# Optimization experiments

Measured on AMD Instinct MI355X. Metric: run time of the kernel, lower is better.

## Reference

```python
import jax, jax.numpy as jnp
from jax import lax
import numpy as np

SIGMA = 25.0
NUM_STEPS = 100
DT = 0.01
SQRT_DT = float(np.sqrt(DT))


def _score(x, eig, t, cond, W1, we, wt, b1, Wc, W2, b2):
    # x: [B,S,H], eig: [B,S], t: scalar, cond: [B,S,H] or None
    h = x @ W1 + eig[..., None] * we + t * wt + b1
    if cond is not None:
        h = h + cond @ Wc
    h = jax.nn.silu(h)
    return h @ W2 + b2


def _diffuse(x_T, eigvals, eigvecs, cond, params, key):
    # reverse SDE from t=1 to t=0 in NUM_STEPS steps
    ts = jnp.linspace(1.0, 0.0, NUM_STEPS)
    keys = jax.random.split(key, NUM_STEPS)
    VT = jnp.swapaxes(eigvecs, -2, -1)  # [B,S,S]

    def step(x, tk):
        t, k = tk
        x_spec = VT @ x                                   # spectral projection [B,S,H]
        score = _score(x_spec, eigvals, t, cond, *params)
        drift = -(SIGMA ** (2.0 * t)) * score
        noise = jax.random.normal(k, x.shape, x.dtype)
        x_new = x - drift * DT + (SIGMA ** t) * SQRT_DT * noise
        return x_new, None

    x, _ = lax.scan(step, x_T, (ts, keys))
    return x


def _make_net(key, H, scale):
    k = jax.random.split(key, 4)
    return dict(
        W1=jax.random.normal(k[0], (H, H), jnp.float32) * scale,
        we=jax.random.normal(k[1], (H,), jnp.float32) * scale,
        wt=jax.random.normal(k[2], (H,), jnp.float32) * scale,
        b1=jnp.zeros((H,), jnp.float32),
        Wc=jax.random.normal(k[3], (H, H), jnp.float32) * scale,
        W2=jax.random.normal(jax.random.fold_in(key, 99), (H, H), jnp.float32) * scale,
        b2=jnp.zeros((H,), jnp.float32),
    )


def setup_inputs() -> dict:
    key = jax.random.key(0)
    B, S, H = 4, 512, 256
    ks = jax.random.split(key, 9)
    inp = {}
    inp['features_text'] = jax.random.normal(ks[0], (B, S, H), jnp.float32)
    inp['features_audio'] = jax.random.normal(ks[1], (B, S, H), jnp.float32)
    inp['features_visual'] = jax.random.normal(ks[2], (B, S, H), jnp.float32)
    sg = jax.random.normal(ks[3], (B, S, S), jnp.float32)
    inp['speaker_graph'] = 0.5 * (sg + jnp.swapaxes(sg, -2, -1))  # symmetric for eigh
    tg = jax.random.normal(ks[4], (B, S, S), jnp.float32)
    inp['temporal_graph'] = 0.5 * (tg + jnp.swapaxes(tg, -2, -1))
    # only text modality (index 0) is missing -> diffusion path for text only
    inp['missing_mask'] = jnp.zeros((B, S, 3), bool).at[:, :, 0].set(True)
    inp['x_T'] = jax.random.normal(ks[5], (B, S, H), jnp.float32)
    scale = 1.0 / np.sqrt(H)
    for prefix, k in [('ts', ks[6]), ('tt', ks[7])]:  # text_speaker / text_temporal nets
        net = _make_net(k, H, scale)
        for name, v in net.items():
            inp[f'{prefix}_{name}'] = v
    kr = jax.random.split(ks[8], 2)
    inp['rec_W'] = jax.random.normal(kr[0], (H, H), jnp.float32) * scale
    inp['rec_b'] = jnp.zeros((H,), jnp.float32)
    return inp


def reference(features_text, features_audio, features_visual,
              speaker_graph, temporal_graph, missing_mask, x_T,
              ts_W1, ts_we, ts_wt, ts_b1, ts_Wc, ts_W2, ts_b2,
              tt_W1, tt_we, tt_wt, tt_b1, tt_Wc, tt_W2, tt_b2,
              rec_W, rec_b):
    # spectral decomposition of both graphs
    s_vals, s_vecs = jnp.linalg.eigh(speaker_graph)
    t_vals, t_vecs = jnp.linalg.eigh(temporal_graph)

    feats = {'text': features_text, 'audio': features_audio, 'visual': features_visual}
    miss = np.asarray(missing_mask)  # concrete branching as in torch forward
    any_missing = [bool(miss[:, :, i].any()) for i in range(3)]

    params = {'text': (
        (ts_W1, ts_we, ts_wt, ts_b1, ts_Wc, ts_W2, ts_b2),
        (tt_W1, tt_we, tt_wt, tt_b1, tt_Wc, tt_W2, tt_b2))}
    key = jax.random.key(42)

    recovered = {}
    for i, modality in enumerate(['text', 'audio', 'visual']):
        if any_missing[i]:
            # condition = mean of present (non-missing) other modalities
            cond_feats = [feats[m] for j, m in enumerate(['text', 'audio', 'visual'])
                          if m != modality and not any_missing[j]]
            cond = None
            if cond_feats:
                cond = jnp.mean(jnp.stack(cond_feats, axis=-1), axis=-1)
            k_s, k_t = jax.random.split(jax.random.fold_in(key, i))
            p_s, p_t = params[modality]
            x_s = _diffuse(x_T, s_vals, s_vecs, cond, p_s, k_s)
            x_t = _diffuse(x_T, t_vals, t_vecs, cond, p_t, k_t)
            rec = 0.5 * (x_s + x_t)
            recovered[modality] = rec @ rec_W + rec_b
        else:
            recovered[modality] = feats[modality]
    return (recovered['text'], recovered['audio'], recovered['visual'])
```

## Files before the change

### kernel.cpp

```cpp
#include <hip/hip_runtime.h>
#include <math.h>
#include <stdint.h>


#define NT 256
#define SZF 131072
#define MATSZ 262144
#define NB 16
#define ILAST 384
#define TBASE (ILAST+1)
#define TSZ (512-TBASE)

#define BD_DK   0
#define BD_ZK   4096
#define BD_RZK  8192
#define BD_TAU  12288
#define BD_DS   16384
#define BD_RHO  20480
#define BD_KSK  20736
#define BD_KIDX 22784
#define BD_DIDX 24832
#define BD_PERM 26880
#define BD_CNT  28928

#define ALD(p)    __hip_atomic_load((p),  __ATOMIC_RELAXED, __HIP_MEMORY_SCOPE_AGENT)
#define AST(p,v)  __hip_atomic_store((p), (v), __ATOMIC_RELAXED, __HIP_MEMORY_SCOPE_AGENT)

__host__ __device__ static inline unsigned rotl32(unsigned v, int r){ return (v<<r)|(v>>(32-r)); }

__host__ __device__ static inline void tf2x32(unsigned k0, unsigned k1,
                                              unsigned x0, unsigned x1,
                                              unsigned* o0, unsigned* o1){
  unsigned ks2 = k0 ^ k1 ^ 0x1BD11BDAu;
  x0 += k0; x1 += k1;
#define TF4(r0,r1,r2,r3) \
  x0 += x1; x1 = rotl32(x1,r0); x1 ^= x0; \
  x0 += x1; x1 = rotl32(x1,r1); x1 ^= x0; \
  x0 += x1; x1 = rotl32(x1,r2); x1 ^= x0; \
  x0 += x1; x1 = rotl32(x1,r3); x1 ^= x0;
  TF4(13,15,26,6)  x0 += k1;  x1 += ks2 + 1u;
  TF4(17,29,16,24) x0 += ks2; x1 += k0 + 2u;
  TF4(13,15,26,6)  x0 += k0;  x1 += k1 + 3u;
  TF4(17,29,16,24) x0 += k1;  x1 += ks2 + 4u;
  TF4(13,15,26,6)  x0 += ks2; x1 += k0 + 5u;
#undef TF4
  *o0 = x0; *o1 = x1;
}

__device__ static inline float erfinv_xla(float x){
  float w = -log1pf(-x*x);
  float p;
  if (w < 5.0f){
    w -= 2.5f;
    p = 2.81022636e-08f;
    p = fmaf(p, w, 3.43273939e-07f);
    p = fmaf(p, w, -3.5233877e-06f);
    p = fmaf(p, w, -4.39150654e-06f);
    p = fmaf(p, w, 0.00021858087f);
    p = fmaf(p, w, -0.00125372503f);
    p = fmaf(p, w, -0.00417768164f);
    p = fmaf(p, w, 0.246640727f);
    p = fmaf(p, w, 1.50140941f);
  } else {
    w = sqrtf(w) - 3.0f;
    p = -0.000200214257f;
    p = fmaf(p, w, 0.000100950558f);
    p = fmaf(p, w, 0.00134934322f);
    p = fmaf(p, w, -0.00367342844f);
    p = fmaf(p, w, 0.00573950773f);
    p = fmaf(p, w, -0.0076224613f);
    p = fmaf(p, w, 0.00943887047f);
    p = fmaf(p, w, 1.00167406f);
    p = fmaf(p, w, 2.83297682f);
  }
  return p*x;
}

__device__ static inline float bits_to_normal(unsigned bits){
  const float MINV = -0.99999994f;
  float f = __uint_as_float((bits >> 9) | 0x3f800000u) - 1.0f;
  float u = fmaxf(MINV, fmaf(f, 2.0f, MINV));
  return 1.41421356237309515f * erfinv_xla(u);
}

__device__ __forceinline__ void gbar2(unsigned* slots, int sg, int g, unsigned epoch,
                                      int* sdead){
  __threadfence_block();
  __syncthreads();
  int t = threadIdx.x;
  if (t == 0) AST(slots + (sg*NB + g)*16, epoch);
  if (t < NB && !*sdead){
    unsigned* sl = slots + (sg*NB + t)*16;
    int spins = 0;
    while (ALD(sl) < epoch){
      __builtin_amdgcn_s_sleep(1);
      if (++spins > (1<<24)){ *sdead = 1; break; }
    }
  }
  __syncthreads();
}

__global__ __launch_bounds__(256) void k_sytd2_lds(const float* Gs, const float* Gt,
                                                   double* Vb, double* smalls,
                                                   unsigned* slots, double* Atail){
  int sg = blockIdx.x / NB, g = blockIdx.x % NB;
  const float* G = (sg < 4) ? (Gs + (size_t)sg*MATSZ) : (Gt + (size_t)(sg-4)*MATSZ);
  double* V = Vb + (size_t)sg*MATSZ;
  double* d  = smalls + (size_t)sg*512;
  double* e  = smalls + 4096 + (size_t)sg*512;
  double* tu = smalls + 8192 + (size_t)sg*512;
  double* acc0 = smalls + 274688 + (size_t)sg*512;
  double* acc1 = acc0 + 4096;
  double* col0 = smalls + 282880 + (size_t)sg*512;
  double* col1 = col0 + 4096;
  double* vvh  = smalls + 291072 + (size_t)sg*512;
  double* At = Atail + (size_t)sg*MATSZ;
  int t = threadIdx.x, wave = t >> 6, lane = t & 63;

  __shared__ double Arows[32][512];
  __shared__ double vv[512], wv[512], col2[512], acc[512];
  __shared__ double red[4];
  __shared__ double bc[4];
  __shared__ int sdead;

  if (t == 0) sdead = 0;

  for (int j=0; j<32; j++){
    int r = NB*j + g;
    for (int c=t; c<512; c+=256)
      Arows[j][c] = (double)G[(size_t)r*512 + c];
  }

  for (int r=t; r<512; r+=256) col2[r] = (r>=1) ? (double)G[(size_t)r*512] : 0.0;
  __syncthreads();
  {
    double part = 0.0;
    for (int r=2+t; r<512; r+=256) part += col2[r]*col2[r];
    #pragma unroll
    for (int off=32; off; off>>=1) part += __shfl_down(part, off, 64);
    if (lane==0) red[wave]=part;
    __syncthreads();
    if (t==0){
      double xsq = red[0]+red[1]+red[2]+red[3];
      double alpha = col2[1];
      double beta,tv,scal;
      if (xsq == 0.0){ beta=alpha; tv=0.0; scal=0.0; }
      else {
        beta = -copysign(sqrt(alpha*alpha + xsq), alpha);
        tv = (beta - alpha)/beta;
        scal = 1.0/(alpha - beta);
      }
      if (g==0){ e[0]=beta; tu[0]=tv; }
      bc[0]=tv; bc[1]=scal;
    }
  }
  __syncthreads();
  double tauv = bc[0];
  {
    double scal = bc[1];
    for (int r=t; r<512; r+=256){
      double v = 0.0;
      if (r==1) v = 1.0;
      else if (r>1) v = (tauv==0.0) ? 0.0 : col2[r]*scal;
      vv[r]=v;
      if (r>=1 && (r & (NB-1))==g) V[r] = v;
    }
  }
  __syncthreads();
  if (g==0){
    for (int r=1+t; r<512; r+=256) AST(&col0[r], (double)G[(size_t)r*512 + 1]);
  }
  {
    int r0 = 1 + ((g - 1) & (NB-1));
    for (int r = r0 + NB*wave; r < 512; r += 4*NB){
      const double* Ar = Arows[r>>4];
      double p = 0.0;
      for (int c=lane; c<512; c+=64) p += Ar[c]*vv[c];
      #pragma unroll
      for (int off=32; off; off>>=1) p += __shfl_down(p, off, 64);
      if (lane==0) AST(&acc0[r], p);
    }
  }

  for (int i=0; i<ILAST; i++){
    gbar2(slots, sg, g, (unsigned)(i+1), &sdead);
    int lo=i+1, lo2=i+2;
    double* accR = (i&1) ? acc1 : acc0;
    double* colR = (i&1) ? col1 : col0;
    double* accW = (i&1) ? acc0 : acc1;
    double* colW = (i&1) ? col0 : col1;
    double part = 0.0;
    for (int r=lo+t; r<512; r+=256){
      double a_ = ALD(&accR[r]);
      double c_ = ALD(&colR[r]);
      acc[r]=a_; col2[r]=c_;
      part += (tauv*a_)*vv[r];
    }
    #pragma unroll
    for (int off=32; off; off>>=1) part += __shfl_down(part, off, 64);
    if (lane==0) red[wave]=part;
    __syncthreads();
    {
      double dot = red[0]+red[1]+red[2]+red[3];
      double alpha2 = -0.5*tauv*dot;
      double vlo = vv[lo];
      double wlo = fma(alpha2, vlo, tauv*acc[lo]);
      for (int r=lo+t; r<512; r+=256){
        double wr = fma(alpha2, vv[r], tauv*acc[r]);
        wv[r]=wr;
        col2[r] = col2[r] - vv[r]*wlo - wr*vlo;
      }
    }
    __syncthreads();
    part = 0.0;
    for (int r=lo2+1+t; r<512; r+=256) part += col2[r]*col2[r];
    #pragma unroll
    for (int off=32; off; off>>=1) part += __shfl_down(part, off, 64);
    if (lane==0) red[wave]=part;
    __syncthreads();
    double tau2, scal2;
    {
      double xsq = red[0]+red[1]+red[2]+red[3];
      double alpha = col2[lo2];
      double beta;
      if (xsq == 0.0){ beta=alpha; tau2=0.0; scal2=0.0; }
      else {
        beta = -copysign(sqrt(alpha*alpha + xsq), alpha);
        tau2 = (beta - alpha)/beta;
        scal2 = 1.0/(alpha - beta);
      }
      if (t==0 && g==0){ e[lo]=beta; tu[lo]=tau2; }
    }
    {
      double vvc[8], wvc[8], v2c[8];
      #pragma unroll
      for (int j=0;j<8;j++){
        int c = lo + lane + 64*j;
        bool ok = c < 512;
        vvc[j] = ok ? vv[c] : 0.0;
        wvc[j] = ok ? wv[c] : 0.0;
        double v2v = 0.0;
        if (ok){
          if (c==lo2) v2v = 1.0;
          else if (c>lo2) v2v = (tau2==0.0) ? 0.0 : col2[c]*scal2;
        }
        v2c[j] = v2v;
      }
      int r0 = lo + ((g - lo) & (NB-1));
      for (int r = r0 + NB*wave; r < 512; r += 4*NB){
        double* Ar = Arows[r>>4];
        double vr = vv[r], wr = wv[r];
        double p = 0.0;
        #pragma unroll
        for (int j=0;j<8;j++){
          int c = lo + lane + 64*j;
          if (c < 512){
            double an = Ar[c] - vr*wvc[j] - wr*vvc[j];
            Ar[c] = an;
            p += an * v2c[j];
            if (c == lo2) AST(&colW[r], an);
          }
        }
        #pragma unroll
        for (int off=32; off; off>>=1) p += __shfl_down(p, off, 64);
        if (lane==0) AST(&accW[r], p);
      }
    }
    __syncthreads();
    for (int r=t; r<512; r+=256){
      double v = 0.0;
      if (r==lo2) v = 1.0;
      else if (r>lo2) v = (tau2==0.0) ? 0.0 : col2[r]*scal2;
      vv[r]=v;
      if (r>=lo2 && (r & (NB-1))==g) V[(size_t)lo*512 + r] = v;
    }
    tauv = tau2;
  }

  if (t < 32){
    int r = NB*t + g;
    if (r <= ILAST) d[r] = Arows[t][r];
  }
  for (int j=0; j<32; j++){
    int r = NB*j + g;
    if (r >= TBASE){
      for (int c=TBASE+t; c<512; c+=256)
        At[(size_t)r*512 + c] = Arows[j][c];
    }
  }
  if (g==0){
    for (int r=t; r<512; r+=256) vvh[r] = vv[r];
  }
}

__global__ __launch_bounds__(256) void k_sy_tail(const double* Atail, double* Vb,
                                                 double* smalls){
  int sg = blockIdx.x;
  double* V = Vb + (size_t)sg*MATSZ;
  double* d  = smalls + (size_t)sg*512;
  double* e  = smalls + 4096 + (size_t)sg*512;
  double* tu = smalls + 8192 + (size_t)sg*512;
  const double* accG = smalls + 274688 + (size_t)sg*512;
  const double* colG = smalls + 282880 + (size_t)sg*512;
  const double* vvG  = smalls + 291072 + (size_t)sg*512;
  const double* At0 = Atail + (size_t)sg*MATSZ;
  int t = threadIdx.x, wave = t >> 6, lane = t & 63;

  __shared__ double At[TSZ*128];
  __shared__ double vv[512], wv[512], col2[512], acc[512], accN[512], colN[512];
  __shared__ double red[4];

  for (int rl=0; rl<TSZ; rl++)
    for (int cl=t; cl<TSZ; cl+=256)
      At[rl*128+cl] = At0[(size_t)(TBASE+rl)*512 + TBASE+cl];
  for (int r=t; r<512; r+=256){
    if (r >= ILAST){ vv[r]=vvG[r]; acc[r]=accG[r]; col2[r]=colG[r]; }
  }
  double tauv = tu[ILAST];
  __syncthreads();

  for (int i=ILAST; i<510; i++){
    int lo=i+1, lo2=i+2;
    double part = 0.0;
    for (int r=lo+t; r<512; r+=256) part += (tauv*acc[r])*vv[r];
    #pragma unroll
    for (int off=32; off; off>>=1) part += __shfl_down(part, off, 64);
    if (lane==0) red[wave]=part;
    __syncthreads();
    {
      double dot = red[0]+red[1]+red[2]+red[3];
      double alpha2 = -0.5*tauv*dot;
      double vlo = vv[lo];
      double wlo = fma(alpha2, vlo, tauv*acc[lo]);
      for (int r=lo+t; r<512; r+=256){
        double wr = fma(alpha2, vv[r], tauv*acc[r]);
        wv[r]=wr;
        col2[r] = col2[r] - vv[r]*wlo - wr*vlo;
      }
    }
    __syncthreads();
    part = 0.0;
    for (int r=lo2+1+t; r<512; r+=256) part += col2[r]*col2[r];
    #pragma unroll
    for (int off=32; off; off>>=1) part += __shfl_down(part, off, 64);
    if (lane==0) red[wave]=part;
    __syncthreads();
    double tau2, scal2;
    {
      double xsq = red[0]+red[1]+red[2]+red[3];
      double alpha = col2[lo2];
      double beta;
      if (xsq == 0.0){ beta=alpha; tau2=0.0; scal2=0.0; }
      else {
        beta = -copysign(sqrt(alpha*alpha + xsq), alpha);
        tau2 = (beta - alpha)/beta;
        scal2 = 1.0/(alpha - beta);
      }
      if (t==0){ e[lo]=beta; tu[lo]=tau2; }
    }
    {
      double vvc[8], wvc[8], v2c[8];
      #pragma unroll
      for (int j=0;j<8;j++){
        int c = lo + lane + 64*j;
        bool ok = c < 512;
        vvc[j] = ok ? vv[c] : 0.0;
        wvc[j] = ok ? wv[c] : 0.0;
        double v2v = 0.0;
        if (ok){
          if (c==lo2) v2v = 1.0;
          else if (c>lo2) v2v = (tau2==0.0) ? 0.0 : col2[c]*scal2;
        }
        v2c[j] = v2v;
      }
      for (int r = lo + wave; r < 512; r += 4){
        double* Ar = &At[(r-TBASE)*128];
        double vr = vv[r], wr = wv[r];
        double p = 0.0;
        #pragma unroll
        for (int j=0;j<8;j++){
          int c = lo + lane + 64*j;
          if (c < 512){
            double an = Ar[c-TBASE] - vr*wvc[j] - wr*vvc[j];
            Ar[c-TBASE] = an;
            p += an * v2c[j];
            if (c == lo2) colN[r] = an;
          }
        }
        #pragma unroll
        for (int off=32; off; off>>=1) p += __shfl_down(p, off, 64);
        if (lane==0) accN[r] = p;
      }
    }
    __syncthreads();
    for (int r=t; r<512; r+=256){
      if (r >= lo2){
        double v = (r==lo2) ? 1.0 : ((tau2==0.0) ? 0.0 : col2[r]*scal2);
        vv[r]=v;
        V[(size_t)lo*512 + r] = v;
        col2[r] = colN[r];
        acc[r] = accN[r];
      }
    }
    tauv = tau2;
    __syncthreads();
  }
  for (int rl=t; rl<TSZ; rl+=256) d[TBASE+rl] = At[rl*128+rl];
}

__global__ void k_scale(double* smalls, int sbase){
  int sg = sbase + blockIdx.x, t = threadIdx.x;
  double* d = smalls + (size_t)sg*512;
  double* e = smalls + 4096 + (size_t)sg*512;
  __shared__ double red[256];
  double m = 0.0;
  for (int i=t;i<512;i+=256) m = fmax(m, fabs(d[i]));
  for (int i=t;i<511;i+=256) m = fmax(m, fabs(e[i]));
  red[t]=m; __syncthreads();
  for (int off=128; off; off>>=1){ if (t<off) red[t]=fmax(red[t],red[t+off]); __syncthreads(); }
  double org = red[0]; if (org == 0.0) org = 1.0;
  if (t==0) smalls[12288+sg] = org;
  double inv = 1.0/org;
  __syncthreads();
  for (int i=t;i<512;i+=256) d[i] *= inv;
  for (int i=t;i<511;i+=256) e[i] *= inv;
  __syncthreads();
  if (t < 31){
    int k = t + 1;
    double ae = fabs(e[16*k - 1]);
    d[16*k - 1] -= ae;
    d[16*k]     -= ae;
  }
}

__global__ __launch_bounds__(256) void k_leaves(double* smalls, double* Zb, int sbase){
  __shared__ double LA[4][256];
  __shared__ double LQ[4][256];
  int t = threadIdx.x, w = t >> 6, lane = t & 63;
  int L = blockIdx.x*4 + w;
  int s_local = L >> 5;
  int sg = sbase + s_local;
  int leaf = L & 31;
  double* dd = smalls + (size_t)sg*512;
  double* ee = smalls + 4096 + (size_t)sg*512;
  double* Z = Zb + (size_t)s_local*MATSZ;
  int base = leaf*16;
  double* A = LA[w]; double* Q = LQ[w];

  for (int i=lane; i<256; i+=64){ A[i]=0.0; Q[i]=0.0; }
  __builtin_amdgcn_sched_barrier(0);
  if (lane < 16){ A[lane*17] = dd[base+lane]; Q[lane*17] = 1.0; }
  if (lane < 15){
    double ev = ee[base+lane];
    A[lane*16+lane+1] = ev; A[(lane+1)*16+lane] = ev;
  }
  __builtin_amdgcn_sched_barrier(0);
  double nr = 0.0;
  if (lane == 0){ for (int i=0;i<256;i++) nr += A[i]*A[i]; }
  nr = __shfl(nr, 0, 64);
  double thr = nr*1e-30 + 1e-300;

  for (int sweep=0; sweep<60; sweep++){
    double offs = 0.0;
    for (int p=0;p<15;p++) for (int q=p+1;q<16;q++){
      double apq = A[p*16+q];
      offs += 2.0*apq*apq;
      if (apq == 0.0) continue;
      double theta = 0.5*(A[q*17]-A[p*17])/apq;
      double tt;
      if (fabs(theta) > 1e18) tt = 0.5/theta;
      else tt = copysign(1.0, theta)/(fabs(theta)+sqrt(theta*theta+1.0));
      double cc = 1.0/sqrt(tt*tt+1.0), ss = tt*cc;
      __builtin_amdgcn_sched_barrier(0);
      if (lane < 16){
        int k = lane;
        double akp=A[k*16+p], akq=A[k*16+q];
        A[k*16+p] = cc*akp - ss*akq;
        A[k*16+q] = ss*akp + cc*akq;
      }
      __builtin_amdgcn_sched_barrier(0);
      if (lane < 16){
        int k = lane;
        double apk=A[p*16+k], aqk=A[q*16+k];
        A[p*16+k] = cc*apk - ss*aqk;
        A[q*16+k] = ss*apk + cc*aqk;
      }
      __builtin_amdgcn_sched_barrier(0);
      if (lane < 16){
        int k = lane;
        double qkp=Q[k*16+p], qkq=Q[k*16+q];
        Q[k*16+p] = cc*qkp - ss*qkq;
        Q[k*16+q] = ss*qkp + cc*qkq;
      }
      __builtin_amdgcn_sched_barrier(0);
    }
    if (offs < thr) break;
  }
  __builtin_amdgcn_sched_barrier(0);
  if (lane == 0){
    for (int i=0;i<16;i++){
      int mi=i;
      for (int j=i+1;j<16;j++) if (A[j*17] < A[mi*17]) mi=j;
      if (mi!=i){
        double tmp=A[i*17]; A[i*17]=A[mi*17]; A[mi*17]=tmp;
        for (int k=0;k<16;k++){ double q1=Q[k*16+i]; Q[k*16+i]=Q[k*16+mi]; Q[k*16+mi]=q1; }
      }
    }
  }
  __builtin_amdgcn_sched_barrier(0);
  if (lane < 16) dd[base+lane] = A[lane*17];
  for (int i=lane; i<256; i+=64){
    int r = i >> 4, c = i & 15;
    Z[(size_t)(base+r)*512 + base + c] = Q[i];
  }
}

__global__ __launch_bounds__(256) void k_deflate(double* smalls, const double* Zsrc_b,
                                                 double* bscr, int level, int sbase){
  const double EPS32 = 5.9604644775390625e-8;
  const double ISQ2  = 0.70710678118654752440;
  int s_local = blockIdx.x;
  int sg = sbase + s_local;
  int hh = 16 << level, n = hh << 1;
  int merge = blockIdx.y, start = merge*n;
  double* d = smalls + (size_t)sg*512;
  const double* e = smalls + 4096 + (size_t)sg*512;
  const double* Z = Zsrc_b + (size_t)s_local*MATSZ;
  double* rotg = smalls + 12544 + (size_t)(sg*32+merge)*1024;
  double* dkG  = bscr + BD_DK  + (size_t)s_local*512 + start;
  double* zkG  = bscr + BD_ZK  + (size_t)s_local*512 + start;
  double* rzkG = bscr + BD_RZK + (size_t)s_local*512 + start;
  double* dsG  = bscr + BD_DS  + (size_t)s_local*512 + start;
  double* rhoG = bscr + BD_RHO;
  int* kidxG = (int*)(bscr + BD_KIDX) + s_local*512 + start;
  int* didxG = (int*)(bscr + BD_DIDX) + s_local*512 + start;
  int* permG = (int*)(bscr + BD_PERM) + s_local*512 + start;
  int* cntG  = (int*)(bscr + BD_CNT) + (s_local*32+merge)*2;

  __shared__ double ds[512], zl[512];
  __shared__ double rc[256], rs[256];
  __shared__ double red[256];
  __shared__ double sv[2];
  __shared__ int perm[512], kidx[512], didx[512];
  __shared__ int rp[256], rq[256];
  __shared__ int counts[2];
  int t = threadIdx.x;
  if (t == 0){
    int i=0, j=hh, k=0;
    while (i < hh && j < n){
      if (d[start+i] <= d[start+j]) perm[k++]=i++; else perm[k++]=j++;
    }
    while (i < hh) perm[k++]=i++;
    while (j < n)  perm[k++]=j++;
  }
  __syncthreads();
  double eb = e[start+hh-1];
  double rho = 2.0*fabs(eb);
  double sgn = (eb < 0.0) ? -1.0 : 1.0;
  for (int i=t; i<n; i+=NT){
    int p = perm[i];
    ds[i] = d[start+p];
    double zr = (p < hh) ? Z[(size_t)(start+hh-1)*512 + start + p]
                         : sgn * Z[(size_t)(start+hh)*512 + start + p];
    zl[i] = zr * ISQ2;
  }
  __syncthreads();
  double m = 0.0;
  for (int i=t;i<n;i+=NT) m = fmax(m, fabs(zl[i]));
  red[t]=m; __syncthreads();
  for (int off=128; off; off>>=1){ if (t<off) red[t]=fmax(red[t],red[t+off]); __syncthreads(); }
  if (t==0) sv[0] = red[0];
  __syncthreads();
  m = 0.0;
  for (int i=t;i<n;i+=NT) m = fmax(m, fabs(ds[i]));
  red[t]=m; __syncthreads();
  for (int off=128; off; off>>=1){ if (t<off) red[t]=fmax(red[t],red[t+off]); __syncthreads(); }
  if (t==0) sv[1] = red[0];
  __syncthreads();
  double zmaxv = sv[0];
  double tol = 8.0*EPS32*fmax(sv[1], zmaxv);

  if (t == 0){
    int K=0, nd=0, nrot=0;
    if (rho*zmaxv <= tol){
      for (int j=0;j<n;j++) didx[nd++]=j;
    } else {
      int pj = -1;
      for (int j=0;j<n;j++){
        if (rho*fabs(zl[j]) <= tol){
          didx[nd++]=j;
        } else if (pj < 0){
          pj = j;
        } else {
          double s_ = zl[pj], c_ = zl[j];
          double tau2 = sqrt(c_*c_ + s_*s_);
          double tdf = ds[j] - ds[pj];
          double cc = c_/tau2, sr = -s_/tau2;
          if (fabs(tdf*cc*sr) <= tol){
            zl[j] = tau2; zl[pj] = 0.0;
            if (nrot < 256){
              rp[nrot]=perm[pj]; rq[nrot]=perm[j]; rc[nrot]=cc; rs[nrot]=sr; nrot++;
            }
            double tn = ds[pj]*cc*cc + ds[j]*sr*sr;
            ds[j]  = ds[pj]*sr*sr + ds[j]*cc*cc;
            ds[pj] = tn;
            didx[nd++] = pj;
            pj = j;
          } else {
            kidx[K++] = pj;
            pj = j;
          }
        }
      }
      if (pj >= 0) kidx[K++] = pj;
    }
    for (int a=1;a<nd;a++){
      int v = didx[a]; double dv = ds[v]; int b = a-1;
      while (b >= 0 && ds[didx[b]] > dv){ didx[b+1]=didx[b]; b--; }
      didx[b+1] = v;
    }
    counts[0]=K; counts[1]=nd;
    cntG[0]=K; cntG[1]=nd;
    rhoG[s_local*32+merge] = rho;
    rotg[0] = (double)nrot;
    for (int i=0;i<nrot;i++){
      rotg[1+4*i]=(double)rp[i]; rotg[2+4*i]=(double)rq[i];
      rotg[3+4*i]=rc[i]; rotg[4+4*i]=rs[i];
    }
  }
  __syncthreads();
  int K = counts[0], nd = counts[1];
  for (int k=t; k<K; k+=NT){
    int ki = kidx[k];
    double dv = ds[ki], zv = zl[ki];
    dkG[k]=dv; zkG[k]=zv; rzkG[k]=(rho*zv)*zv; kidxG[k]=ki;
  }
  for (int j=t; j<n;  j+=NT){ dsG[j]=ds[j]; permG[j]=perm[j]; }
  for (int j=t; j<nd; j+=NT) didxG[j]=didx[j];
}

__global__ __launch_bounds__(256) void k_bisect(double* bscr, int level, int split){
  int s_local = blockIdx.x;
  int hh = 16 << level, n = hh << 1;
  int merge = blockIdx.y, start = merge*n;
  const double* dkG  = bscr + BD_DK  + (size_t)s_local*512 + start;
  const double* zkG  = bscr + BD_ZK  + (size_t)s_local*512 + start;
  const double* rzkG = bscr + BD_RZK + (size_t)s_local*512 + start;
  double* taukG = bscr + BD_TAU + (size_t)s_local*512 + start;
  int* KskG = (int*)(bscr + BD_KSK) + s_local*512 + start;
  const int* cntG = (int*)(bscr + BD_CNT) + (s_local*32+merge)*2;
  double rho = (bscr + BD_RHO)[s_local*32+merge];
  __shared__ double dks[512], rzks[512], zks[512];
  int t = threadIdx.x;
  int K = cntG[0];
  for (int i=t;i<K;i+=NT){ dks[i]=dkG[i]; rzks[i]=rzkG[i]; zks[i]=zkG[i]; }
  __syncthreads();
  int lane = t & 63, w = t >> 6;
  for (int j2 = blockIdx.z*4 + w; j2 < K; j2 += split*4){
    int Kb; double lo, hi;
    if (j2 < K-1){
      double mid = 0.5*(dks[j2+1]-dks[j2]);
      double dj = dks[j2];
      double part = 0.0;
      for (int i=lane;i<K;i+=64){ double dif=(dks[i]-dj)-mid; part += rzks[i]/dif; }
      #pragma unroll
      for (int off=32; off; off>>=1) part += __shfl_xor(part, off, 64);
      double gg = 1.0 + part;
      if (gg >= 0.0){ Kb=j2;   lo=0.0;  hi=mid; }
      else          { Kb=j2+1; lo=-mid; hi=0.0; }
    } else {
      double part = 0.0;
      for (int i=lane;i<K;i+=64) part += zks[i]*zks[i];
      #pragma unroll
      for (int off=32; off; off>>=1) part += __shfl_xor(part, off, 64);
      Kb=K-1; lo=0.0; hi=rho*part + 1e-300;
    }
    double dK = dks[Kb];
    for (int it=0; it<72; it++){
      double mid = 0.5*(lo+hi);
      if (mid==lo || mid==hi) break;
      double part = 0.0;
      for (int i=lane;i<K;i+=64){ double dif=(dks[i]-dK)-mid; part += rzks[i]/dif; }
      #pragma unroll
      for (int off=32; off; off>>=1) part += __shfl_xor(part, off, 64);
      double gg = 1.0 + part;
      if (gg < 0.0) lo=mid; else hi=mid;
    }
    if (lane==0){ KskG[j2]=Kb; taukG[j2]=0.5*(lo+hi); }
  }
}

__global__ __launch_bounds__(256) void k_sfin(double* smalls, double* Sm_b,
                                              const double* bscr, int level, int sbase){
  int s_local = blockIdx.x;
  int sg = sbase + s_local;
  int hh = 16 << level, n = hh << 1;
  int merge = blockIdx.y, start = merge*n;
  double* d = smalls + (size_t)sg*512;
  double* Sm = Sm_b + (size_t)s_local*MATSZ;
  const double* dkG  = bscr + BD_DK  + (size_t)s_local*512 + start;
  const double* zkG  = bscr + BD_ZK  + (size_t)s_local*512 + start;
  const double* taukG= bscr + BD_TAU + (size_t)s_local*512 + start;
  const double* dsG  = bscr + BD_DS  + (size_t)s_local*512 + start;
  const int* KskG = (int*)(bscr + BD_KSK) + s_local*512 + start;
  const int* kidxG= (int*)(bscr + BD_KIDX) + s_local*512 + start;
  const int* didxG= (int*)(bscr + BD_DIDX) + s_local*512 + start;
  const int* permG= (int*)(bscr + BD_PERM) + s_local*512 + start;
  const int* cntG = (int*)(bscr + BD_CNT) + (s_local*32+merge)*2;
  double rho = (bscr + BD_RHO)[s_local*32+merge];
  __shared__ double dk[512], zk[512], tauk[512], zh[512], outlam[512], ds[512];
  __shared__ int Ksk[512], kidx[512], didx[512], perm[512], outid[512];
  int t = threadIdx.x;
  int K = cntG[0], nd = cntG[1];
  for (int i=t;i<K;i+=NT){
    dk[i]=dkG[i]; zk[i]=zkG[i]; tauk[i]=taukG[i]; Ksk[i]=KskG[i]; kidx[i]=kidxG[i];
  }
  for (int i=t;i<n;i+=NT){ ds[i]=dsG[i]; perm[i]=permG[i]; }
  for (int i=t;i<nd;i+=NT) didx[i]=didxG[i];
  __syncthreads();
  for (int i=t; i<K; i+=NT){
    double P = (Ksk[i]==i) ? tauk[i] : (dk[Ksk[i]]-dk[i]) + tauk[i];
    for (int j=0;j<K;j++){
      if (j==i) continue;
      double num = (dk[Ksk[j]]-dk[i]) + tauk[j];
      double den = dk[j]-dk[i];
      P *= num/den;
    }
    zh[i] = copysign(sqrt(fabs(P/rho)), zk[i]);
  }
  __syncthreads();
  if (t == 0){
    int a=0, b=0;
    for (int j=0;j<n;j++){
      double la = (a<K)  ? (dk[Ksk[a]]+tauk[a]) : 1e300;
      double lb = (b<nd) ? ds[didx[b]]          : 1e300;
      if (la <= lb){ outid[j]=a;     outlam[j]=la; a++; }
      else         { outid[j]=512+b; outlam[j]=lb; b++; }
    }
  }
  __syncthreads();
  for (int j=t; j<n; j+=NT) d[start+j] = outlam[j];
  for (int j=t; j<n; j+=NT){
    double* col = Sm + (size_t)(start+j)*512;
    int id = outid[j];
    for (int i=0;i<n;i++) col[i]=0.0;
    if (id >= 512){
      col[perm[didx[id-512]]] = 1.0;
    } else {
      int k = id;
      double ss_ = 0.0;
      for (int i=0;i<K;i++){
        double dif = (dk[i]-dk[Ksk[k]]) - tauk[k];
        if (dif == 0.0) dif = 1e-300;
        double v = zh[i]/dif;
        col[perm[kidx[i]]] = v; ss_ += v*v;
      }
      double inv = 1.0/sqrt(ss_);
      for (int i=0;i<K;i++) col[perm[kidx[i]]] *= inv;
    }
  }
}

__global__ __launch_bounds__(256) void k_rot(double* Sm_b, const double* smalls,
                                             int level, int sbase){
  int s_local = blockIdx.x, merge = blockIdx.y;
  int sg = sbase + s_local;
  int hh = 16 << level, n = hh << 1, start = merge*n;
  const double* rotg = smalls + 12544 + (size_t)(sg*32+merge)*1024;
  double* Sm = Sm_b + (size_t)s_local*MATSZ;
  int cnt = (int)rotg[0];
  for (int i=cnt-1; i>=0; i--){
    int p = (int)rotg[1+4*i], q = (int)rotg[2+4*i];
    double c = rotg[3+4*i], sr = rotg[4+4*i];
    for (int j=threadIdx.x; j<n; j+=256){
      double* col = Sm + (size_t)(start+j)*512;
      double a = col[p], b = col[q];
      col[p] = c*a - sr*b;
      col[q] = sr*a + c*b;
    }
    __syncthreads();
  }
}

__global__ __launch_bounds__(256) void k_gemm64(const double* Zsrc_b, const double* Sm_b,
                                                double* Zdst_b, int level){
  int hh = 16 << level, n = hh << 1;
  int mpm = 512 / n;
  int bz = blockIdx.z;
  int s = bz / mpm, merge = bz % mpm;
  int start = merge*n;
  const double* Zs = Zsrc_b + (size_t)s*MATSZ;
  const double* Sm = Sm_b + (size_t)s*MATSZ;
  double* Zd = Zdst_b + (size_t)s*MATSZ;
  int row0 = start + blockIdx.y*32, col0 = start + blockIdx.x*32;
  int t = threadIdx.x;
  int tr = t >> 4, tc = t & 15;
  __shared__ double As[32][33];
  __shared__ double Bs[32][33];
  double a00=0,a01=0,a10=0,a11=0;
  for (int q0=0; q0<n; q0+=32){
    #pragma unroll
    for (int it=0; it<4; it++){
      int idx = t + it*256;
      int r = idx >> 5, q = idx & 31;
      As[r][q] = Zs[(size_t)(row0+r)*512 + start + q0 + q];
    }
    #pragma unroll
    for (int it=0; it<4; it++){
      int idx = t + it*256;
      int c = idx >> 5, q = idx & 31;
      Bs[q][c] = Sm[(size_t)(col0+c)*512 + q0 + q];
    }
    __syncthreads();
    #pragma unroll 8
    for (int q=0;q<32;q++){
      double ar0=As[tr][q], ar1=As[tr+16][q];
      double bc0=Bs[q][tc], bc1=Bs[q][tc+16];
      a00 = fma(ar0,bc0,a00); a01 = fma(ar0,bc1,a01);
      a10 = fma(ar1,bc0,a10); a11 = fma(ar1,bc1,a11);
    }
    __syncthreads();
  }
  Zd[(size_t)(row0+tr)*512 + col0+tc]       = a00;
  Zd[(size_t)(row0+tr)*512 + col0+tc+16]    = a01;
  Zd[(size_t)(row0+tr+16)*512 + col0+tc]    = a10;
  Zd[(size_t)(row0+tr+16)*512 + col0+tc+16] = a11;
}

__global__ __launch_bounds__(256) void k_backq(double* Z2_b, const double* Vh_b,
                                               const double* smalls, int sbase){
  int s_local = blockIdx.x, cb = blockIdx.y;
  int sg = sbase + s_local;
  double* Z = Z2_b + (size_t)s_local*MATSZ;
  const double* V = Vh_b + (size_t)sg*MATSZ;
  const double* tu = smalls + 8192 + (size_t)sg*512;
  int cg = threadIdx.x >> 5, lane = threadIdx.x & 31;
  int c = cb*8 + cg;
  __shared__ double zc[8][512];
  for (int r=lane; r<512; r+=32) zc[cg][r] = Z[(size_t)r*512 + c];
  for (int i=509; i>=0; i--){
    double tv = tu[i];
    if (tv == 0.0) continue;
    double wp = 0.0;
    for (int r=i+1+lane; r<512; r+=32) wp += V[(size_t)i*512 + r]*zc[cg][r];
    #pragma unroll
    for (int off=16; off; off>>=1) wp += __shfl_down(wp, off, 32);
    double w = __shfl(wp, 0, 32);
    double tw = tv*w;
    for (int r=i+1+lane; r<512; r+=32) zc[cg][r] -= tw*V[(size_t)i*512 + r];
  }
  for (int r=lane; r<512; r+=32) Z[(size_t)r*512 + c] = zc[cg][r];
}

__global__ void k_finalize(const double* Z2_b, const double* smalls,
                           float* Vs32, float* Vt32, float* eig, int sbase){
  int s_local = blockIdx.x;
  int sg = sbase + s_local;
  const double* Z = Z2_b + (size_t)s_local*MATSZ;
  float* Vt_pass = (sg < 4) ? (Vs32 + (size_t)sg*MATSZ)
                            : (Vt32 + (size_t)(sg-4)*MATSZ);
  double org = smalls[12288+sg];
  int idx = blockIdx.y*256 + threadIdx.x;
  int r = idx >> 9, c = idx & 511;
  Vt_pass[(size_t)c*512 + r] = (float)Z[(size_t)r*512 + c];
  if (idx < 512)
    eig[(size_t)sg*512 + idx] = (float)(smalls[(size_t)sg*512 + idx]*org);
}

struct KArgs {
  const float* Vt;
  const float* Vt2;
  float *xspec, *hbuf, *x, *E;
  const float *W1s, *W1t, *W2s, *W2t;
  const float *b2s, *b2t, *wts, *wtt, *b1s, *b1t, *wes, *wet;
  const float *cond, *Wcs, *Wct;
  const float *eig;
  const float *rec, *recW, *recb;
  float* out;
  float t, a, bc;
  unsigned nk0, nk1, nk2, nk3;
  int mode, nmat, ntx;
};

__global__ __launch_bounds__(256) void k_gemm32(KArgs P){
  int t = threadIdx.x;
  int L = blockIdx.x;
  int mat = L % P.nmat;
  int tile = L / P.nmat;
  int n0 = (tile % P.ntx) << 5;
  int m0 = (tile / P.ntx) << 6;
  const float *A, *B; float *C;
  int lda, K, chain = 0;
  if (P.mode == 0){
    A = (mat < 4) ? (P.Vt + (size_t)mat*MATSZ) : (P.Vt2 + (size_t)(mat-4)*MATSZ);
    lda = 512; K = 512;
    B = P.x + (size_t)mat*SZF; C = P.xspec + (size_t)mat*SZF;
  } else if (P.mode == 1){
    chain = mat >> 2;
    A = P.xspec + (size_t)mat*SZF; lda = 256; K = 256;
    B = chain ? P.W1t : P.W1s; C = P.hbuf + (size_t)mat*SZF;
  } else if (P.mode == 2){
    chain = mat >> 2;
    A = P.hbuf + (size_t)mat*SZF; lda = 256; K = 256;
    B = chain ? P.W2t : P.W2s; C = P.x + (size_t)mat*SZF;
  } else if (P.mode == 3){
    chain = mat;
    A = P.cond; lda = 256; K = 256;
    B = chain ? P.Wct : P.Wcs; C = P.E + (size_t)chain*4*SZF;
  } else {
    A = P.rec; lda = 256; K = 256;
    B = P.recW; C = P.out;
  }
  __shared__ float As[2][32][68];
  __shared__ float Bs[2][32][36];
  float acc[4][2] = {{0}};
  const int ra = t >> 2, kk4 = (t & 3) << 2;
  const int kb = (t & 127) >> 3, c4 = (t & 7) << 2;
  const int tr4 = (t >> 4) << 2, tc2 = (t & 15) << 1;
  const float* Aptr = &A[(size_t)(m0 + ra)*lda + kk4];
  const float* Bptr = &B[(size_t)kb*256 + n0 + c4];
  {
    const float4 av  = *(const float4*)Aptr;
    const float4 av2 = *(const float4*)(Aptr + 16);
    As[0][kk4+0][ra]=av.x;  As[0][kk4+1][ra]=av.y;  As[0][kk4+2][ra]=av.z;  As[0][kk4+3][ra]=av.w;
    As[0][16+kk4+0][ra]=av2.x; As[0][16+kk4+1][ra]=av2.y; As[0][16+kk4+2][ra]=av2.z; As[0][16+kk4+3][ra]=av2.w;
    if (t < 128){
      const float4 bv  = *(const float4*)Bptr;
      const float4 bv2 = *(const float4*)(Bptr + (size_t)16*256);
      *(float4*)&Bs[0][kb][c4] = bv;
      *(float4*)&Bs[0][kb+16][c4] = bv2;
    }
  }
  int buf = 0;
  for (int k0=0; k0<K; k0+=32){
    __syncthreads();
    bool more = (k0+32) < K;
    float4 avN, avN2, bvN, bvN2;
    if (more){
      avN  = *(const float4*)(Aptr + k0 + 32);
      avN2 = *(const float4*)(Aptr + k0 + 48);
      if (t < 128){
        bvN  = *(const float4*)(Bptr + (size_t)(k0+32)*256);
        bvN2 = *(const float4*)(Bptr + (size_t)(k0+48)*256);
      }
    }
    {
      const float (*Asb)[68] = As[buf];
      const float (*Bsb)[36] = Bs[buf];
      #pragma unroll
      for (int kk=0; kk<32; kk++){
        const float4 a4 = *(const float4*)&Asb[kk][tr4];
        const float2 b2 = *(const float2*)&Bsb[kk][tc2];
        const float ar[4] = {a4.x, a4.y, a4.z, a4.w};
        #pragma unroll
        for (int q=0;q<4;q++){
          acc[q][0] = fmaf(ar[q], b2.x, acc[q][0]);
          acc[q][1] = fmaf(ar[q], b2.y, acc[q][1]);
        }
      }
    }
    if (more){
      int nb = buf^1;
      As[nb][kk4+0][ra]=avN.x;  As[nb][kk4+1][ra]=avN.y;  As[nb][kk4+2][ra]=avN.z;  As[nb][kk4+3][ra]=avN.w;
      As[nb][16+kk4+0][ra]=avN2.x; As[nb][16+kk4+1][ra]=avN2.y; As[nb][16+kk4+2][ra]=avN2.z; As[nb][16+kk4+3][ra]=avN2.w;
      if (t < 128){
        *(float4*)&Bs[nb][kb][c4] = bvN;
        *(float4*)&Bs[nb][kb+16][c4] = bvN2;
      }
      buf = nb;
    }
  }
  #pragma unroll
  for (int q=0;q<4;q++){
    int r = m0 + tr4 + q;
    size_t rowoff = (size_t)r*256 + n0 + tc2;
    float2 cv;
    if (P.mode == 2) cv = *(const float2*)&C[rowoff];
    float res[2];
    #pragma unroll
    for (int p=0;p<2;p++){
      int c = n0 + tc2 + p;
      size_t oi = (size_t)r*256 + c;
      float v = acc[q][p];
      if (P.mode == 1){
        v += P.E[(size_t)mat*SZF + oi] + P.t * ((chain ? P.wtt : P.wts)[c]);
        float sg = 1.0f/(1.0f + expf(-v));
        v = v * sg;
      } else if (P.mode == 2){
        float bias = (chain ? P.b2t : P.b2s)[c];
        unsigned j = ((unsigned)(mat & 3))*131072u + (unsigned)oi;
        unsigned kk0 = chain ? P.nk2 : P.nk0;
        unsigned kk1 = chain ? P.nk3 : P.nk1;
        unsigned y0, y1;
        tf2x32(kk0, kk1, 0u, j, &y0, &y1);
        float nz = bits_to_normal(y0 ^ y1);
        float cx = (p==0) ? cv.x : cv.y;
        v = cx + P.a*(v + bias) + P.bc*nz;
      } else if (P.mode == 3){
        int bb = r >> 9, s2 = r & 511;
        v += (chain ? P.b1t : P.b1s)[c]
           + P.eig[(size_t)(chain*4 + bb)*512 + s2] * ((chain ? P.wet : P.wes)[c]);
      } else if (P.mode == 4){
        v += P.recb[c];
      }
      res[p] = v;
    }
    *(float2*)&C[rowoff] = make_float2(res[0], res[1]);
  }
}

__global__ void k_init(float* cond, float* x, const float* a, const float* v,
                       const float* xT){
  size_t i = (size_t)blockIdx.x*256 + threadIdx.x;
  size_t b = i >> 17, off = i & 131071;
  x[i] = xT[((b & 3) << 17) + off];
  if (i < 524288) cond[i] = 0.5f*(a[i] + v[i]);
}

__global__ void k_recc(float* rec, const float* x, float* out,
                       const float* a, const float* v){
  size_t i = (size_t)blockIdx.x*256 + threadIdx.x;
  if (i < 524288) rec[i] = 0.5f*(x[i] + x[i + 524288]);
  out[524288 + i] = (i < 524288) ? a[i] : v[i - 524288];
}

extern "C" void kernel_launch(void* const* d_in, const int* in_sizes, int n_in,
                              void* d_out, int out_size, void* d_ws, size_t ws_size,
                              hipStream_t stream){
  const float* f_audio   = (const float*)d_in[1];
  const float* f_visual  = (const float*)d_in[2];
  const float* g_speaker = (const float*)d_in[3];
  const float* g_temporal= (const float*)d_in[4];
  const float* x_T       = (const float*)d_in[6];
  const float* tsW1=(const float*)d_in[7],  *tswe=(const float*)d_in[8],
             * tswt=(const float*)d_in[9],  *tsb1=(const float*)d_in[10],
             * tsWc=(const float*)d_in[11], *tsW2=(const float*)d_in[12],
             * tsb2=(const float*)d_in[13];
  const float* ttW1=(const float*)d_in[14], *ttwe=(const float*)d_in[15],
             * ttwt=(const float*)d_in[16], *ttb1=(const float*)d_in[17],
             * ttWc=(const float*)d_in[18], *ttW2=(const float*)d_in[19],
             * ttb2=(const float*)d_in[20];
  const float* recW=(const float*)d_in[21], *recb=(const float*)d_in[22];
  float* out = (float*)d_out;

  const size_t MB = 1ull << 20;
  if (ws_size < 43*MB) return;
  bool wide = ws_size >= 80*MB;

  char* ws = (char*)d_ws;
  double* Vh     = (double*)(ws + 0);
  double* Atail  = (double*)(ws + 16*MB);
  double* A64    = (double*)(ws + 16*MB);
  double* Zb     = wide ? (double*)(ws + 48*MB) : (double*)(ws + 24*MB);
  double* Sm     = wide ? (double*)(ws + 64*MB) : (double*)(ws + 32*MB);
  double* smalls = (double*)(ws + 40*MB);
  unsigned* slots = (unsigned*)(smalls + 295168);
  float* Vt32_s  = (float*)(ws + 0);
  float* Vt32_t  = (float*)(ws + 8*MB);
  float* eig32   = (float*)(ws + 42*MB + 512*1024);
  double* bscr   = (double*)(ws + 42*MB + 640*1024);
  float* cond  = (float*)(ws + 16*MB);
  float* E     = (float*)(ws + 18*MB);
  float* xall  = (float*)(ws + 22*MB);
  float* xspec = (float*)(ws + 26*MB);
  float* hbuf  = (float*)(ws + 30*MB);

  unsigned f0, f1;
  tf2x32(0u, 42u, 0u, 0u, &f0, &f1);
  unsigned s0,s1,t0,t1;
  tf2x32(f0, f1, 0u, 0u, &s0, &s1);
  tf2x32(f0, f1, 0u, 1u, &t0, &t1);
  unsigned skeys[100][2], tkeys[100][2];
  for (int k=0; k<100; k++){
    tf2x32(s0, s1, 0u, (unsigned)k, &skeys[k][0], &skeys[k][1]);
    tf2x32(t0, t1, 0u, (unsigned)k, &tkeys[k][0], &tkeys[k][1]);
  }

  hipMemsetAsync(slots, 0, 16384, stream);

  k_sytd2_lds<<<8*NB, 256, 0, stream>>>(g_speaker, g_temporal, Vh, smalls, slots, Atail);
  k_sy_tail<<<8, 256, 0, stream>>>(Atail, Vh, smalls);

  int npass = wide ? 1 : 2;
  int nmat  = wide ? 8 : 4;
  for (int pass=0; pass<npass; pass++){
    int sbase = wide ? 0 : 4*pass;
    k_scale<<<nmat, 256, 0, stream>>>(smalls, sbase);
    hipMemsetAsync(Zb, 0, (size_t)(wide?16:8)*MB, stream);
    hipMemsetAsync(A64, 0, (size_t)(wide?16:8)*MB, stream);
    k_leaves<<<nmat*8, 256, 0, stream>>>(smalls, Zb, sbase);
    for (int level=0; level<5; level++){
      int n = 32 << level, mpm = 512/n;
      double* src = (level & 1) ? A64 : Zb;
      double* dst = (level & 1) ? Zb  : A64;
      int split = 2 << level;
      k_deflate<<<dim3(nmat, mpm), 256, 0, stream>>>(smalls, src, bscr, level, sbase);
      k_bisect<<<dim3(nmat, mpm, split), 256, 0, stream>>>(bscr, level, split);
      k_sfin<<<dim3(nmat, mpm), 256, 0, stream>>>(smalls, Sm, bscr, level, sbase);
      k_rot<<<dim3(nmat, mpm), 256, 0, stream>>>(Sm, smalls, level, sbase);
      k_gemm64<<<dim3(n/32, n/32, nmat*mpm), 256, 0, stream>>>(src, Sm, dst, level);
    }
    k_backq<<<dim3(nmat, 64), 256, 0, stream>>>(A64, Vh, smalls, sbase);
    k_finalize<<<dim3(nmat, 1024), 256, 0, stream>>>(A64, smalls,
                                                     Vt32_s, Vt32_t, eig32, sbase);
  }

  k_init<<<4096, 256, 0, stream>>>(cond, xall, f_audio, f_visual, x_T);

  KArgs P;
  P.Vt = Vt32_s; P.Vt2 = Vt32_t;
  P.xspec = xspec; P.hbuf = hbuf; P.x = xall; P.E = E;
  P.W1s = tsW1; P.W1t = ttW1; P.W2s = tsW2; P.W2t = ttW2;
  P.b2s = tsb2; P.b2t = ttb2; P.wts = tswt; P.wtt = ttwt;
  P.b1s = tsb1; P.b1t = ttb1; P.wes = tswe; P.wet = ttwe;
  P.cond = cond; P.Wcs = tsWc; P.Wct = ttWc;
  P.eig = eig32; P.rec = xspec; P.recW = recW; P.recb = recb; P.out = out;
  P.t = 0.f; P.a = 0.f; P.bc = 0.f;
  P.nk0 = 0; P.nk1 = 0; P.nk2 = 0; P.nk3 = 0;
  P.ntx = 8;

  P.mode = 3; P.nmat = 2;
  k_gemm32<<<512, 256, 0, stream>>>(P);

  for (int k=0; k<100; k++){
    float tf = (float)(1.0 - (double)k/99.0);
    float av = (float)(pow(25.0, 2.0*(double)tf) * 0.01);
    float bcv = (float)(pow(25.0, (double)tf) * 0.1);
    P.nk0 = skeys[k][0]; P.nk1 = skeys[k][1];
    P.nk2 = tkeys[k][0]; P.nk3 = tkeys[k][1];
    P.nmat = 8;
    P.mode = 0;
    k_gemm32<<<512, 256, 0, stream>>>(P);
    P.mode = 1; P.t = tf;
    k_gemm32<<<512, 256, 0, stream>>>(P);
    P.mode = 2; P.a = av; P.bc = bcv;
    k_gemm32<<<512, 256, 0, stream>>>(P);
  }

  k_recc<<<4096, 256, 0, stream>>>(xspec, xall, out, f_audio, f_visual);
  P.mode = 4; P.nmat = 1;
  k_gemm32<<<256, 256, 0, stream>>>(P);
}
```

Measured before the change: 14.13 ms.

## Fuse per-step spectral projection, score MLP and SDE update into one kernel

```diff
diff --git a/kernel.cpp b/kernel.cpp
--- a/kernel.cpp
+++ b/kernel.cpp
@@ -868,17 +868,12 @@
 }
 
 struct KArgs {
-  const float* Vt;
-  const float* Vt2;
-  float *xspec, *hbuf, *x, *E;
-  const float *W1s, *W1t, *W2s, *W2t;
-  const float *b2s, *b2t, *wts, *wtt, *b1s, *b1t, *wes, *wet;
   const float *cond, *Wcs, *Wct;
+  const float *b1s, *b1t, *wes, *wet;
   const float *eig;
   const float *rec, *recW, *recb;
+  float *E;
   float* out;
-  float t, a, bc;
-  unsigned nk0, nk1, nk2, nk3;
   int mode, nmat, ntx;
 };
 
@@ -890,27 +885,16 @@
   int n0 = (tile % P.ntx) << 5;
   int m0 = (tile / P.ntx) << 6;
   const float *A, *B; float *C;
-  int lda, K, chain = 0;
-  if (P.mode == 0){
-    A = (mat < 4) ? (P.Vt + (size_t)mat*MATSZ) : (P.Vt2 + (size_t)(mat-4)*MATSZ);
-    lda = 512; K = 512;
-    B = P.x + (size_t)mat*SZF; C = P.xspec + (size_t)mat*SZF;
-  } else if (P.mode == 1){
-    chain = mat >> 2;
-    A = P.xspec + (size_t)mat*SZF; lda = 256; K = 256;
-    B = chain ? P.W1t : P.W1s; C = P.hbuf + (size_t)mat*SZF;
-  } else if (P.mode == 2){
-    chain = mat >> 2;
-    A = P.hbuf + (size_t)mat*SZF; lda = 256; K = 256;
-    B = chain ? P.W2t : P.W2s; C = P.x + (size_t)mat*SZF;
-  } else if (P.mode == 3){
+  int chain = 0;
+  if (P.mode == 3){
     chain = mat;
-    A = P.cond; lda = 256; K = 256;
+    A = P.cond;
     B = chain ? P.Wct : P.Wcs; C = P.E + (size_t)chain*4*SZF;
   } else {
-    A = P.rec; lda = 256; K = 256;
+    A = P.rec;
     B = P.recW; C = P.out;
   }
+  const int lda = 256, K = 256;
   __shared__ float As[2][32][68];
   __shared__ float Bs[2][32][36];
   float acc[4][2] = {{0}};
@@ -974,38 +958,226 @@
   for (int q=0;q<4;q++){
     int r = m0 + tr4 + q;
     size_t rowoff = (size_t)r*256 + n0 + tc2;
-    float2 cv;
-    if (P.mode == 2) cv = *(const float2*)&C[rowoff];
     float res[2];
     #pragma unroll
     for (int p=0;p<2;p++){
       int c = n0 + tc2 + p;
-      size_t oi = (size_t)r*256 + c;
       float v = acc[q][p];
-      if (P.mode == 1){
-        v += P.E[(size_t)mat*SZF + oi] + P.t * ((chain ? P.wtt : P.wts)[c]);
-        float sg = 1.0f/(1.0f + expf(-v));
-        v = v * sg;
-      } else if (P.mode == 2){
-        float bias = (chain ? P.b2t : P.b2s)[c];
-        unsigned j = ((unsigned)(mat & 3))*131072u + (unsigned)oi;
-        unsigned kk0 = chain ? P.nk2 : P.nk0;
-        unsigned kk1 = chain ? P.nk3 : P.nk1;
-        unsigned y0, y1;
-        tf2x32(kk0, kk1, 0u, j, &y0, &y1);
-        float nz = bits_to_normal(y0 ^ y1);
-        float cx = (p==0) ? cv.x : cv.y;
-        v = cx + P.a*(v + bias) + P.bc*nz;
-      } else if (P.mode == 3){
+      if (P.mode == 3){
         int bb = r >> 9, s2 = r & 511;
         v += (chain ? P.b1t : P.b1s)[c]
            + P.eig[(size_t)(chain*4 + bb)*512 + s2] * ((chain ? P.wet : P.wes)[c]);
-      } else if (P.mode == 4){
+      } else {
         v += P.recb[c];
       }
       res[p] = v;
     }
     *(float2*)&C[rowoff] = make_float2(res[0], res[1]);
+  }
+}
+
+struct KStep {
+  const float *Vt, *Vt2, *xr;
+  float* xw;
+  const float *W1s, *W1t, *W2s, *W2t;
+  const float *b2s, *b2t, *wts, *wtt;
+  const float *E;
+  float t, a, bc;
+  unsigned nk0, nk1, nk2, nk3;
+};
+
+__global__ __launch_bounds__(256) void k_step(KStep S){
+  int t = threadIdx.x;
+  int mat = blockIdx.x & 7;
+  int row0 = (blockIdx.x >> 3) << 4;
+  int chain = mat >> 2;
+  const float* Vt = (mat < 4) ? (S.Vt + (size_t)mat*MATSZ) : (S.Vt2 + (size_t)(mat-4)*MATSZ);
+  const float* xr = S.xr + (size_t)mat*SZF;
+  float*       xw = S.xw + (size_t)mat*SZF;
+  const float* W1 = chain ? S.W1t : S.W1s;
+  const float* W2 = chain ? S.W2t : S.W2s;
+  const float* Eb = S.E + (size_t)mat*SZF;
+  const float* wt = chain ? S.wtt : S.wts;
+  const float* b2 = chain ? S.b2t : S.b2s;
+
+  __shared__ float Bt[2][16][260];
+  __shared__ float Av[2][16][20];
+  __shared__ float xsp[16][260];
+  __shared__ float hl[16][260];
+
+  const int r0 = (t >> 6) << 2;
+  const int c4 = (t & 63) << 2;
+  const int kb = t & 15, cb = (t >> 4) << 4;
+  const int ar = t >> 2, ak4 = (t & 3) << 2;
+
+  float acc[4][4];
+  float4 pb[4]; float4 pa;
+
+  #pragma unroll
+  for (int i=0;i<4;i++)
+    #pragma unroll
+    for (int j=0;j<4;j++) acc[i][j]=0.f;
+  #pragma unroll
+  for (int j=0;j<4;j++) pb[j] = *(const float4*)&xr[(size_t)kb*256 + cb + 4*j];
+  if (t < 64) pa = *(const float4*)&Vt[(size_t)(row0+ar)*512 + ak4];
+  #pragma unroll
+  for (int j=0;j<4;j++) *(float4*)&Bt[0][kb][cb+4*j] = pb[j];
+  if (t < 64){
+    Av[0][ak4+0][ar]=pa.x; Av[0][ak4+1][ar]=pa.y; Av[0][ak4+2][ar]=pa.z; Av[0][ak4+3][ar]=pa.w;
+  }
+  int cur = 0;
+  for (int k0=0; k0<512; k0+=16){
+    __syncthreads();
+    bool more = (k0+16) < 512;
+    if (more){
+      #pragma unroll
+      for (int j=0;j<4;j++)
+        pb[j] = *(const float4*)&xr[(size_t)(k0+16+kb)*256 + cb + 4*j];
+      if (t < 64) pa = *(const float4*)&Vt[(size_t)(row0+ar)*512 + k0+16 + ak4];
+    }
+    #pragma unroll
+    for (int kk=0; kk<16; kk++){
+      const float4 b = *(const float4*)&Bt[cur][kk][c4];
+      #pragma unroll
+      for (int i=0;i<4;i++){
+        float a = Av[cur][kk][r0+i];
+        acc[i][0] = fmaf(a, b.x, acc[i][0]);
+        acc[i][1] = fmaf(a, b.y, acc[i][1]);
+        acc[i][2] = fmaf(a, b.z, acc[i][2]);
+        acc[i][3] = fmaf(a, b.w, acc[i][3]);
+      }
+    }
+    if (more){
+      int nb = cur^1;
+      #pragma unroll
+      for (int j=0;j<4;j++) *(float4*)&Bt[nb][kb][cb+4*j] = pb[j];
+      if (t < 64){
+        Av[nb][ak4+0][ar]=pa.x; Av[nb][ak4+1][ar]=pa.y; Av[nb][ak4+2][ar]=pa.z; Av[nb][ak4+3][ar]=pa.w;
+      }
+      cur = nb;
+    }
+  }
+  #pragma unroll
+  for (int i=0;i<4;i++)
+    *(float4*)&xsp[r0+i][c4] = make_float4(acc[i][0],acc[i][1],acc[i][2],acc[i][3]);
+  __syncthreads();
+
+  #pragma unroll
+  for (int i=0;i<4;i++)
+    #pragma unroll
+    for (int j=0;j<4;j++) acc[i][j]=0.f;
+  #pragma unroll
+  for (int j=0;j<4;j++) pb[j] = *(const float4*)&W1[(size_t)kb*256 + cb + 4*j];
+  #pragma unroll
+  for (int j=0;j<4;j++) *(float4*)&Bt[0][kb][cb+4*j] = pb[j];
+  cur = 0;
+  for (int k0=0; k0<256; k0+=16){
+    __syncthreads();
+    bool more = (k0+16) < 256;
+    if (more){
+      #pragma unroll
+      for (int j=0;j<4;j++)
+        pb[j] = *(const float4*)&W1[(size_t)(k0+16+kb)*256 + cb + 4*j];
+    }
+    #pragma unroll
+    for (int kk=0; kk<16; kk++){
+      const float4 b = *(const float4*)&Bt[cur][kk][c4];
+      #pragma unroll
+      for (int i=0;i<4;i++){
+        float a = xsp[r0+i][k0+kk];
+        acc[i][0] = fmaf(a, b.x, acc[i][0]);
+        acc[i][1] = fmaf(a, b.y, acc[i][1]);
+        acc[i][2] = fmaf(a, b.z, acc[i][2]);
+        acc[i][3] = fmaf(a, b.w, acc[i][3]);
+      }
+    }
+    if (more){
+      int nb = cur^1;
+      #pragma unroll
+      for (int j=0;j<4;j++) *(float4*)&Bt[nb][kb][cb+4*j] = pb[j];
+      cur = nb;
+    }
+  }
+  {
+    float tv = S.t;
+    #pragma unroll
+    for (int i=0;i<4;i++){
+      int rg = row0 + r0 + i;
+      const float4 ev = *(const float4*)&Eb[(size_t)rg*256 + c4];
+      float res[4];
+      #pragma unroll
+      for (int j=0;j<4;j++){
+        int c = c4 + j;
+        float v = acc[i][j];
+        v += ((const float*)&ev)[j] + tv * wt[c];
+        float sg = 1.0f/(1.0f + expf(-v));
+        res[j] = v * sg;
+      }
+      *(float4*)&hl[r0+i][c4] = make_float4(res[0],res[1],res[2],res[3]);
+    }
+  }
+  __syncthreads();
+
+  #pragma unroll
+  for (int i=0;i<4;i++)
+    #pragma unroll
+    for (int j=0;j<4;j++) acc[i][j]=0.f;
+  #pragma unroll
+  for (int j=0;j<4;j++) pb[j] = *(const float4*)&W2[(size_t)kb*256 + cb + 4*j];
+  #pragma unroll
+  for (int j=0;j<4;j++) *(float4*)&Bt[0][kb][cb+4*j] = pb[j];
+  cur = 0;
+  for (int k0=0; k0<256; k0+=16){
+    __syncthreads();
+    bool more = (k0+16) < 256;
+    if (more){
+      #pragma unroll
+      for (int j=0;j<4;j++)
+        pb[j] = *(const float4*)&W2[(size_t)(k0+16+kb)*256 + cb + 4*j];
+    }
+    #pragma unroll
+    for (int kk=0; kk<16; kk++){
+      const float4 b = *(const float4*)&Bt[cur][kk][c4];
+      #pragma unroll
+      for (int i=0;i<4;i++){
+        float a = hl[r0+i][k0+kk];
+        acc[i][0] = fmaf(a, b.x, acc[i][0]);
+        acc[i][1] = fmaf(a, b.y, acc[i][1]);
+        acc[i][2] = fmaf(a, b.z, acc[i][2]);
+        acc[i][3] = fmaf(a, b.w, acc[i][3]);
+      }
+    }
+    if (more){
+      int nb = cur^1;
+      #pragma unroll
+      for (int j=0;j<4;j++) *(float4*)&Bt[nb][kb][cb+4*j] = pb[j];
+      cur = nb;
+    }
+  }
+  {
+    unsigned kk0 = chain ? S.nk2 : S.nk0;
+    unsigned kk1 = chain ? S.nk3 : S.nk1;
+    #pragma unroll
+    for (int i=0;i<4;i++){
+      int rg = row0 + r0 + i;
+      const float4 cv = *(const float4*)&xr[(size_t)rg*256 + c4];
+      float res[4];
+      #pragma unroll
+      for (int j=0;j<4;j++){
+        int c = c4 + j;
+        unsigned oi = (unsigned)rg*256u + (unsigned)c;
+        float v = acc[i][j];
+        float bias = b2[c];
+        unsigned jj = ((unsigned)(mat & 3))*131072u + oi;
+        unsigned y0, y1;
+        tf2x32(kk0, kk1, 0u, jj, &y0, &y1);
+        float nz = bits_to_normal(y0 ^ y1);
+        float cx = ((const float*)&cv)[j];
+        v = cx + S.a*(v + bias) + S.bc*nz;
+        res[j] = v;
+      }
+      *(float4*)&xw[(size_t)rg*256 + c4] = make_float4(res[0],res[1],res[2],res[3]);
+    }
   }
 }
 
@@ -1061,9 +1233,9 @@
   double* bscr   = (double*)(ws + 42*MB + 640*1024);
   float* cond  = (float*)(ws + 16*MB);
   float* E     = (float*)(ws + 18*MB);
-  float* xall  = (float*)(ws + 22*MB);
+  float* xb0   = (float*)(ws + 22*MB);
   float* xspec = (float*)(ws + 26*MB);
-  float* hbuf  = (float*)(ws + 30*MB);
+  float* xb1   = (float*)(ws + 30*MB);
 
   unsigned f0, f1;
   tf2x32(0u, 42u, 0u, 0u, &f0, &f1);
@@ -1105,39 +1277,35 @@
                                                      Vt32_s, Vt32_t, eig32, sbase);
   }
 
-  k_init<<<4096, 256, 0, stream>>>(cond, xall, f_audio, f_visual, x_T);
+  k_init<<<4096, 256, 0, stream>>>(cond, xb0, f_audio, f_visual, x_T);
 
   KArgs P;
-  P.Vt = Vt32_s; P.Vt2 = Vt32_t;
-  P.xspec = xspec; P.hbuf = hbuf; P.x = xall; P.E = E;
-  P.W1s = tsW1; P.W1t = ttW1; P.W2s = tsW2; P.W2t = ttW2;
-  P.b2s = tsb2; P.b2t = ttb2; P.wts = tswt; P.wtt = ttwt;
+  P.cond = cond; P.Wcs = tsWc; P.Wct = ttWc;
   P.b1s = tsb1; P.b1t = ttb1; P.wes = tswe; P.wet = ttwe;
-  P.cond = cond; P.Wcs = tsWc; P.Wct = ttWc;
-  P.eig = eig32; P.rec = xspec; P.recW = recW; P.recb = recb; P.out = out;
-  P.t = 0.f; P.a = 0.f; P.bc = 0.f;
-  P.nk0 = 0; P.nk1 = 0; P.nk2 = 0; P.nk3 = 0;
-  P.ntx = 8;
-
-  P.mode = 3; P.nmat = 2;
+  P.eig = eig32; P.E = E;
+  P.rec = xspec; P.recW = recW; P.recb = recb; P.out = out;
+  P.mode = 3; P.nmat = 2; P.ntx = 8;
   k_gemm32<<<512, 256, 0, stream>>>(P);
+
+  KStep S;
+  S.Vt = Vt32_s; S.Vt2 = Vt32_t;
+  S.W1s = tsW1; S.W1t = ttW1; S.W2s = tsW2; S.W2t = ttW2;
+  S.b2s = tsb2; S.b2t = ttb2; S.wts = tswt; S.wtt = ttwt;
+  S.E = E;
 
   for (int k=0; k<100; k++){
     float tf = (float)(1.0 - (double)k/99.0);
     float av = (float)(pow(25.0, 2.0*(double)tf) * 0.01);
     float bcv = (float)(pow(25.0, (double)tf) * 0.1);
-    P.nk0 = skeys[k][0]; P.nk1 = skeys[k][1];
-    P.nk2 = tkeys[k][0]; P.nk3 = tkeys[k][1];
-    P.nmat = 8;
-    P.mode = 0;
-    k_gemm32<<<512, 256, 0, stream>>>(P);
-    P.mode = 1; P.t = tf;
-    k_gemm32<<<512, 256, 0, stream>>>(P);
-    P.mode = 2; P.a = av; P.bc = bcv;
-    k_gemm32<<<512, 256, 0, stream>>>(P);
-  }
-
-  k_recc<<<4096, 256, 0, stream>>>(xspec, xall, out, f_audio, f_visual);
+    S.t = tf; S.a = av; S.bc = bcv;
+    S.nk0 = skeys[k][0]; S.nk1 = skeys[k][1];
+    S.nk2 = tkeys[k][0]; S.nk3 = tkeys[k][1];
+    S.xr = (k & 1) ? xb1 : xb0;
+    S.xw = (k & 1) ? xb0 : xb1;
+    k_step<<<256, 256, 0, stream>>>(S);
+  }
+
+  k_recc<<<4096, 256, 0, stream>>>(xspec, xb0, out, f_audio, f_visual);
   P.mode = 4; P.nmat = 1;
   k_gemm32<<<256, 256, 0, stream>>>(P);
 }
```

Measured after the change: 17.58 ms. +24.5%, slower.
